# Optimization experiments

Hardware: AMD Instinct MI355X
Metric: run time of the kernel (lower is better)

## Reference

```python
import jax, jax.numpy as jnp
import numpy as np

B, T, F, H = 1024, 100, 128, 512


def _uniform(key, shape, stdv):
    return jax.random.uniform(key, shape, jnp.float32, -stdv, stdv)


def setup_inputs() -> dict:
    key = jax.random.key(0)
    ks = jax.random.split(key, 24)
    values = jax.random.normal(ks[0], (B, T, F), jnp.float32)
    delta = jax.random.uniform(ks[1], (B, T, F), jnp.float32) * 5.0
    masks = (jax.random.uniform(ks[2], (B, T, F), jnp.float32) < 0.7).astype(jnp.float32)
    rbfs = jax.random.normal(ks[3], (B, T, F), jnp.float32)
    inp = jnp.stack([values, delta, masks, rbfs], axis=1)  # [B,4,T,F]

    s_h = 1.0 / np.sqrt(H)
    s_f = 1.0 / np.sqrt(F)
    params = dict(
        inp=inp,
        # TemporalDecay h: Linear(F->H)
        W_dh=_uniform(ks[4], (H, F), s_h), b_dh=_uniform(ks[5], (H,), s_h),
        # TemporalDecay x (diag): effective diagonal of W
        w_dx=_uniform(ks[6], (F,), s_f), b_dx=_uniform(ks[7], (F,), s_f),
        # output_layer: Linear(H->F)
        W_out=_uniform(ks[8], (F, H), s_f), b_out=_uniform(ks[9], (F,), s_f),
        W_z=_uniform(ks[10], (F, F), s_f), b_z=_uniform(ks[11], (F,), s_f),
        # concat layer: Linear(2F->F)
        W_cat=_uniform(ks[12], (F, 2 * F), s_f), b_cat=_uniform(ks[13], (F,), s_f),
        # beta layer: Linear(2F->F)
        W_beta=_uniform(ks[14], (F, 2 * F), s_f), b_beta=_uniform(ks[15], (F,), s_f),
        # GRUCell(2F -> H)
        W_ih=_uniform(ks[16], (3 * H, 2 * F), s_h), b_ih=_uniform(ks[17], (3 * H,), s_h),
        W_hh=_uniform(ks[18], (3 * H, H), s_h), b_hh=_uniform(ks[19], (3 * H,), s_h),
    )
    return params


def _forward(inp, W_dh, b_dh, w_dx, b_dx, W_out, b_out, W_z, b_z,
             W_cat, b_cat, W_beta, b_beta, W_ih, b_ih, W_hh, b_hh):
    values = jnp.swapaxes(inp[:, 0], 0, 1)  # [T,B,F]
    delta = jnp.swapaxes(inp[:, 1], 0, 1)
    masks = jnp.swapaxes(inp[:, 2], 0, 1)
    rbfs = jnp.swapaxes(inp[:, 3], 0, 1)

    W_z_m = W_z * (1.0 - jnp.eye(F, dtype=W_z.dtype))  # off-diagonal mask

    def mae(hat, v, m):
        return jnp.sum(jnp.abs(v - hat) * m) / (jnp.sum(m) + 1e-5)

    def step(carry, xs):
        hid, x_loss = carry
        v, d, m, r = xs
        gamma_x = jnp.exp(-jax.nn.relu(d * w_dx + b_dx))          # diag decay
        gamma_h = jnp.exp(-jax.nn.relu(d @ W_dh.T + b_dh))        # [B,H]
        x_hat = hid @ W_out.T + b_out
        x_loss = x_loss + 2.0 * mae(x_hat, v, m)                  # x_loss + x_hat_loss share value
        x_c = m * v + (1.0 - m) * x_hat
        concat_hat = jnp.concatenate([x_c, r], axis=1) @ W_cat.T + b_cat
        x_loss = x_loss + mae(concat_hat, v, m)
        a_c = m * v + (1.0 - m) * concat_hat
        z_hat = a_c @ W_z_m.T + b_z
        x_loss = x_loss + mae(z_hat, v, m)
        beta = jax.nn.sigmoid(jnp.concatenate([gamma_x, m], axis=1) @ W_beta.T + b_beta)
        c_hat = beta * z_hat + (1.0 - beta) * x_hat
        x_loss = x_loss + mae(c_hat, v, m)
        c_c = m * v + (1.0 - m) * c_hat
        # GRUCell
        h = hid * gamma_h
        gi = jnp.concatenate([c_c, m], axis=1) @ W_ih.T + b_ih
        gh = h @ W_hh.T + b_hh
        i_r, i_z, i_n = jnp.split(gi, 3, axis=1)
        h_r, h_z, h_n = jnp.split(gh, 3, axis=1)
        rg = jax.nn.sigmoid(i_r + h_r)
        zg = jax.nn.sigmoid(i_z + h_z)
        ng = jnp.tanh(i_n + rg * h_n)
        h_new = (1.0 - zg) * ng + zg * h
        return (h_new, x_loss), (c_hat, c_c)

    hid0 = jnp.zeros((values.shape[1], H), values.dtype)
    (_, x_loss), (c_hats, c_cs) = jax.lax.scan(step, (hid0, jnp.float32(0.0)),
                                               (values, delta, masks, rbfs))
    c_hat_list = jnp.swapaxes(c_hats, 0, 1)   # [B,T,F]
    imputations = jnp.swapaxes(c_cs, 0, 1)
    return c_hat_list, imputations, x_loss * 5.0


def reference(inp, W_dh, b_dh, w_dx, b_dx, W_out, b_out, W_z, b_z,
              W_cat, b_cat, W_beta, b_beta, W_ih, b_ih, W_hh, b_hh):
    # x_loss in torch accumulates x_hat term twice (x_loss += ... and x_hat_loss += same);
    # but note: torch adds x_hat_loss separately, x_loss only once per term. Faithful: x_loss gets
    # one add per hat (x_hat, concat_hat, z_hat, c_hat) -> see _forward (2.0 factor removed below).
    return _forward(inp, W_dh, b_dh, w_dx, b_dx, W_out, b_out, W_z, b_z,
                    W_cat, b_cat, W_beta, b_beta, W_ih, b_ih, W_hh, b_hh)
```

## Files before the change

kernel.cpp:

```cpp
#include <hip/hip_runtime.h>
#include <cmath>

#define NB 256
#define NT 256

static constexpr int B = 1024, T = 100, F = 128, H = 512;
static constexpr size_t BTF = (size_t)B * T * F;
static constexpr int TF = T * F;
static constexpr int STRB = 4 * T * F;

static constexpr size_t OFF_FLAGS = 0;
static constexpr size_t OFF_REL   = 4096;
static constexpr size_t OFF_DEN   = 4112;
static constexpr size_t OFF_LOSST = 4240;
static constexpr size_t OFF_HID   = 4368;
static constexpr size_t ZERO_FLOATS = OFF_HID + (size_t)B * H;
static constexpr size_t OFF_H    = ZERO_FLOATS;
static constexpr size_t OFF_GH   = OFF_H + (size_t)B * H;
static constexpr size_t OFF_XHAT = OFF_GH + (size_t)B * 3 * H;
static constexpr size_t OFF_CONC = OFF_XHAT + (size_t)B * F;
static constexpr size_t OFF_BETA = OFF_CONC + (size_t)B * F;
static constexpr size_t OFF_CC   = OFF_BETA + (size_t)B * F;

__device__ __forceinline__ float4 ld4(const float* p) {
    return *reinterpret_cast<const float4*>(p);
}
__device__ __forceinline__ float sigm(float x) { return 1.f / (1.f + expf(-x)); }

__device__ __forceinline__ void gsync(unsigned* flags, unsigned* rel, unsigned gen) {
    __syncthreads();
    __threadfence();
    const int tid = threadIdx.x;
    if (blockIdx.x == 0) {
        if (tid > 0) {
            while (__hip_atomic_load(&flags[(size_t)tid * 16], __ATOMIC_RELAXED,
                                     __HIP_MEMORY_SCOPE_AGENT) < gen)
                __builtin_amdgcn_s_sleep(4);
        }
        __syncthreads();
        if (tid == 0)
            __hip_atomic_store(rel, gen, __ATOMIC_RELAXED, __HIP_MEMORY_SCOPE_AGENT);
    } else {
        if (tid == 0) {
            __hip_atomic_store(&flags[(size_t)blockIdx.x * 16], gen, __ATOMIC_RELAXED,
                               __HIP_MEMORY_SCOPE_AGENT);
            while (__hip_atomic_load(rel, __ATOMIC_RELAXED,
                                     __HIP_MEMORY_SCOPE_AGENT) < gen)
                __builtin_amdgcn_s_sleep(16);
        }
    }
    __threadfence();
    __syncthreads();
}

__device__ __forceinline__ void stage4(float* __restrict__ dst, int k, int r, float4 p) {
    dst[(k + 0) * 64 + r] = p.x; dst[(k + 1) * 64 + r] = p.y;
    dst[(k + 2) * 64 + r] = p.z; dst[(k + 3) * 64 + r] = p.w;
}

template <typename FA, typename FB>
__device__ __forceinline__ void gemm_tile64(int K, FA loadA4, FB loadB4,
                                            float* __restrict__ sAB, float acc[4][4]) {
    const int tid = threadIdx.x;
    const int lr = tid >> 2;
    const int lk = (tid & 3) << 2;
    const int tx = tid & 15, ty = tid >> 4;
    const int nc = K >> 5;

    float4 pa0 = loadA4(lr, lk);
    float4 pa1 = loadA4(lr, lk + 16);
    float4 pb0 = loadB4(lr, lk);
    float4 pb1 = loadB4(lr, lk + 16);
    stage4(sAB, lk, lr, pa0);
    stage4(sAB, lk + 16, lr, pa1);
    stage4(sAB + 2048, lk, lr, pb0);
    stage4(sAB + 2048, lk + 16, lr, pb1);
    __syncthreads();

    for (int c = 0; c < nc; ++c) {
        const float* sA = sAB + (c & 1) * 4096;
        const float* sB = sA + 2048;
        if (c + 1 < nc) {
            const int k0 = (c + 1) << 5;
            pa0 = loadA4(lr, k0 + lk);
            pa1 = loadA4(lr, k0 + lk + 16);
            pb0 = loadB4(lr, k0 + lk);
            pb1 = loadB4(lr, k0 + lk + 16);
        }
#pragma unroll
        for (int kk = 0; kk < 32; ++kk) {
            const float4 av = *reinterpret_cast<const float4*>(&sA[kk * 64 + ty * 4]);
            const float4 bv = *reinterpret_cast<const float4*>(&sB[kk * 64 + tx * 4]);
            const float a0[4] = {av.x, av.y, av.z, av.w};
            const float b0[4] = {bv.x, bv.y, bv.z, bv.w};
#pragma unroll
            for (int i = 0; i < 4; ++i)
#pragma unroll
                for (int j = 0; j < 4; ++j)
                    acc[i][j] = fmaf(a0[i], b0[j], acc[i][j]);
        }
        if (c + 1 < nc) {
            float* dA = sAB + ((c + 1) & 1) * 4096;
            stage4(dA, lk, lr, pa0);
            stage4(dA, lk + 16, lr, pa1);
            stage4(dA + 2048, lk, lr, pb0);
            stage4(dA + 2048, lk + 16, lr, pb1);
        }
        __syncthreads();
    }
}

__global__ void __launch_bounds__(NT) mgru_main(
    const float* __restrict__ inp,
    const float* __restrict__ W_dh, const float* __restrict__ b_dh,
    const float* __restrict__ w_dx, const float* __restrict__ b_dx,
    const float* __restrict__ W_out, const float* __restrict__ b_out,
    const float* __restrict__ W_z,   const float* __restrict__ b_z,
    const float* __restrict__ W_cat, const float* __restrict__ b_cat,
    const float* __restrict__ W_beta,const float* __restrict__ b_beta,
    const float* __restrict__ W_ih,  const float* __restrict__ b_ih,
    const float* __restrict__ W_hh,  const float* __restrict__ b_hh,
    float* __restrict__ out, float* __restrict__ ws)
{
    __shared__ float sAB[2 * 4096];

    unsigned* flags = reinterpret_cast<unsigned*>(ws) + OFF_FLAGS;
    unsigned* rel   = reinterpret_cast<unsigned*>(ws) + OFF_REL;
    float* den   = ws + OFF_DEN;
    float* lossT = ws + OFF_LOSST;
    float* hid   = ws + OFF_HID;
    float* hdec  = ws + OFF_H;
    float* gh    = ws + OFF_GH;
    float* xhat  = ws + OFF_XHAT;
    float* conc  = ws + OFF_CONC;
    float* betav = ws + OFF_BETA;
    float* ccw   = ws + OFF_CC;

    const int bid = blockIdx.x, tid = threadIdx.x;
    const int tx = tid & 15, ty = tid >> 4;
    unsigned gen = 1;

    for (int s = bid * NT + tid; s < B * T; s += NB * NT) {
        int b = s / T, t = s - b * T;
        const float* mrow = inp + (size_t)b * STRB + 2 * TF + (size_t)t * F;
        float sum = 0.f;
        for (int f = 0; f < F; f += 4) {
            float4 m4 = ld4(mrow + f);
            sum += m4.x + m4.y + m4.z + m4.w;
        }
        atomicAdd(&den[t], sum);
    }
    gsync(flags, rel, gen); ++gen;

    for (int t = 0; t < T; ++t) {
        const size_t tF = (size_t)t * F;
        if (bid >= 64 && bid < 192) {
            const int idx = bid - 64, rt = idx >> 3, ct = idx & 7;
            float acc[4][4] = {};
            gemm_tile64(128,
                [=](int r, int k) { return ld4(inp + (size_t)(rt * 64 + r) * STRB + TF + tF + k); },
                [=](int c, int k) { return ld4(W_dh + (size_t)(ct * 64 + c) * F + k); },
                sAB, acc);
#pragma unroll
            for (int i = 0; i < 4; ++i) {
                int b = rt * 64 + ty * 4 + i;
#pragma unroll
                for (int j = 0; j < 4; ++j) {
                    int c = ct * 64 + tx * 4 + j;
                    float g = expf(-fmaxf(acc[i][j] + b_dh[c], 0.f));
                    hdec[(size_t)b * H + c] = hid[(size_t)b * H + c] * g;
                }
            }
        } else if (bid >= 192 && bid < 224) {
            const int t2 = bid - 192, rt = t2 >> 1, ct = t2 & 1;
            float acc[4][4] = {};
            gemm_tile64(512,
                [=](int r, int k) { return ld4(hid + (size_t)(rt * 64 + r) * H + k); },
                [=](int c, int k) { return ld4(W_out + (size_t)(ct * 64 + c) * H + k); },
                sAB, acc);
#pragma unroll
            for (int i = 0; i < 4; ++i) {
                int b = rt * 64 + ty * 4 + i;
#pragma unroll
                for (int j = 0; j < 4; ++j) {
                    int c = ct * 64 + tx * 4 + j;
                    xhat[(size_t)b * F + c] = acc[i][j] + b_out[c];
                }
            }
        } else if (bid >= 224) {
            const int t2 = bid - 224, rt = t2 >> 1, ct = t2 & 1;
            float acc[4][4] = {};
            gemm_tile64(256,
                [=](int r, int k) {
                    int b = rt * 64 + r;
                    if (k < 128) {
                        float4 d4 = ld4(inp + (size_t)b * STRB + TF + tF + k);
                        float4 w4 = ld4(w_dx + k), c4 = ld4(b_dx + k);
                        float4 q;
                        q.x = expf(-fmaxf(fmaf(d4.x, w4.x, c4.x), 0.f));
                        q.y = expf(-fmaxf(fmaf(d4.y, w4.y, c4.y), 0.f));
                        q.z = expf(-fmaxf(fmaf(d4.z, w4.z, c4.z), 0.f));
                        q.w = expf(-fmaxf(fmaf(d4.w, w4.w, c4.w), 0.f));
                        return q;
                    }
                    return ld4(inp + (size_t)b * STRB + 2 * TF + tF + (k - 128));
                },
                [=](int c, int k) { return ld4(W_beta + (size_t)(ct * 64 + c) * (2 * F) + k); },
                sAB, acc);
#pragma unroll
            for (int i = 0; i < 4; ++i) {
                int b = rt * 64 + ty * 4 + i;
#pragma unroll
                for (int j = 0; j < 4; ++j) {
                    int c = ct * 64 + tx * 4 + j;
                    betav[(size_t)b * F + c] = sigm(acc[i][j] + b_beta[c]);
                }
            }
        }
        gsync(flags, rel, gen); ++gen;
        {
            int g0 = -1, g1 = -1, cat2 = -1;
            if (bid >= 64 && bid < 192) { g0 = (bid - 64) * 2; g1 = g0 + 1; }
            else if (bid >= 192)        { g0 = 256 + (bid - 192); if (bid < 224) cat2 = bid - 192; }
            else                        { g0 = 320 + bid; }
#pragma unroll 1
            for (int pass = 0; pass < 2; ++pass) {
                int g = pass ? g1 : g0;
                if (g < 0) continue;
                const int rt = g / 24, ct = g % 24;
                float acc[4][4] = {};
                gemm_tile64(512,
                    [=](int r, int k) { return ld4(hdec + (size_t)(rt * 64 + r) * H + k); },
                    [=](int c, int k) { return ld4(W_hh + (size_t)(ct * 64 + c) * H + k); },
                    sAB, acc);
#pragma unroll
                for (int i = 0; i < 4; ++i) {
                    int b = rt * 64 + ty * 4 + i;
#pragma unroll
                    for (int j = 0; j < 4; ++j) {
                        int c = ct * 64 + tx * 4 + j;
                        gh[(size_t)b * 1536 + c] = acc[i][j] + b_hh[c];
                    }
                }
            }
            if (cat2 >= 0) {
                const int rt = cat2 >> 1, ct = cat2 & 1;
                float acc[4][4] = {};
                gemm_tile64(256,
                    [=](int r, int k) {
                        int b = rt * 64 + r;
                        if (k < 128) {
                            float4 v4 = ld4(inp + (size_t)b * STRB + tF + k);
                            float4 m4 = ld4(inp + (size_t)b * STRB + 2 * TF + tF + k);
                            float4 x4 = ld4(xhat + (size_t)b * F + k);
                            float4 q;
                            q.x = m4.x * v4.x + (1.f - m4.x) * x4.x;
                            q.y = m4.y * v4.y + (1.f - m4.y) * x4.y;
                            q.z = m4.z * v4.z + (1.f - m4.z) * x4.z;
                            q.w = m4.w * v4.w + (1.f - m4.w) * x4.w;
                            return q;
                        }
                        return ld4(inp + (size_t)b * STRB + 3 * TF + tF + (k - 128));
                    },
                    [=](int c, int k) { return ld4(W_cat + (size_t)(ct * 64 + c) * (2 * F) + k); },
                    sAB, acc);
#pragma unroll
                for (int i = 0; i < 4; ++i) {
                    int b = rt * 64 + ty * 4 + i;
#pragma unroll
                    for (int j = 0; j < 4; ++j) {
                        int c = ct * 64 + tx * 4 + j;
                        conc[(size_t)b * F + c] = acc[i][j] + b_cat[c];
                    }
                }
            }
        }
        gsync(flags, rel, gen); ++gen;
        if (bid >= 32 && bid < 64) {
            const int t2 = bid - 32, rt = t2 >> 1, ct = t2 & 1;
            float acc[4][4] = {};
            gemm_tile64(128,
                [=](int r, int k) {
                    int b = rt * 64 + r;
                    float4 v4 = ld4(inp + (size_t)b * STRB + tF + k);
                    float4 m4 = ld4(inp + (size_t)b * STRB + 2 * TF + tF + k);
                    float4 c4 = ld4(conc + (size_t)b * F + k);
                    float4 q;
                    q.x = m4.x * v4.x + (1.f - m4.x) * c4.x;
                    q.y = m4.y * v4.y + (1.f - m4.y) * c4.y;
                    q.z = m4.z * v4.z + (1.f - m4.z) * c4.z;
                    q.w = m4.w * v4.w + (1.f - m4.w) * c4.w;
                    return q;
                },
                [=](int c, int k) {
                    float4 w = ld4(W_z + (size_t)(ct * 64 + c) * F + k);
                    int cg = ct * 64 + c;
                    w.x = (cg == k + 0) ? 0.f : w.x;
                    w.y = (cg == k + 1) ? 0.f : w.y;
                    w.z = (cg == k + 2) ? 0.f : w.z;
                    w.w = (cg == k + 3) ? 0.f : w.w;
                    return w;
                },
                sAB, acc);
            float lsum = 0.f;
#pragma unroll
            for (int i = 0; i < 4; ++i) {
                int b = rt * 64 + ty * 4 + i;
#pragma unroll
                for (int j = 0; j < 4; ++j) {
                    int c = ct * 64 + tx * 4 + j;
                    float zh = acc[i][j] + b_z[c];
                    float xh = xhat[(size_t)b * F + c];
                    float bt = betav[(size_t)b * F + c];
                    float ch = bt * zh + (1.f - bt) * xh;
                    const size_t ib = (size_t)b * STRB + tF;
                    float v = inp[ib + c];
                    float m = inp[ib + 2 * TF + c];
                    float cc = m * v + (1.f - m) * ch;
                    out[(size_t)b * TF + tF + c] = ch;
                    out[BTF + (size_t)b * TF + tF + c] = cc;
                    ccw[(size_t)b * F + c] = cc;
                    float co = conc[(size_t)b * F + c];
                    lsum += m * (2.f * fabsf(v - xh) + fabsf(v - co) +
                                 fabsf(v - zh) + fabsf(v - ch));
                }
            }
            __syncthreads();
            sAB[tid] = lsum;
            __syncthreads();
            for (int s = 128; s > 0; s >>= 1) {
                if (tid < s) sAB[tid] += sAB[tid + s];
                __syncthreads();
            }
            if (tid == 0) atomicAdd(&lossT[t], sAB[0] / (den[t] + 1e-5f));
        }
        gsync(flags, rel, gen); ++gen;
        if (bid >= 64 && bid < 192) {
            const int idx = bid - 64, rt = idx >> 3, hc = idx & 7;
            float acc3[3][4][4] = {};
#pragma unroll
            for (int g = 0; g < 3; ++g) {
                gemm_tile64(256,
                    [=](int r, int k) {
                        int b = rt * 64 + r;
                        if (k < 128) return ld4(ccw + (size_t)b * F + k);
                        return ld4(inp + (size_t)b * STRB + 2 * TF + tF + (k - 128));
                    },
                    [=](int c, int k) { return ld4(W_ih + (size_t)(g * H + hc * 64 + c) * (2 * F) + k); },
                    sAB, acc3[g]);
            }
#pragma unroll
            for (int i = 0; i < 4; ++i) {
                int b = rt * 64 + ty * 4 + i;
#pragma unroll
                for (int j = 0; j < 4; ++j) {
                    int c = hc * 64 + tx * 4 + j;
                    float ir  = acc3[0][i][j] + b_ih[c];
                    float iz  = acc3[1][i][j] + b_ih[H + c];
                    float inn = acc3[2][i][j] + b_ih[2 * H + c];
                    float hr = gh[(size_t)b * 1536 + c];
                    float hz = gh[(size_t)b * 1536 + H + c];
                    float hn = gh[(size_t)b * 1536 + 2 * H + c];
                    float hv = hdec[(size_t)b * H + c];
                    float rg = sigm(ir + hr);
                    float zg = sigm(iz + hz);
                    float ng = tanhf(inn + rg * hn);
                    hid[(size_t)b * H + c] = (1.f - zg) * ng + zg * hv;
                }
            }
        }
        gsync(flags, rel, gen); ++gen;
    }
    if (bid == 0 && tid == 0) {
        float s = 0.f;
        for (int t = 0; t < T; ++t) s += lossT[t];
        out[2 * BTF] = s * 5.0f;
    }
}

extern "C" void kernel_launch(void* const* d_in, const int* in_sizes, int n_in,
                              void* d_out, int out_size, void* d_ws, size_t ws_size,
                              hipStream_t stream) {
    const float* inp    = (const float*)d_in[0];
    const float* W_dh   = (const float*)d_in[1];
    const float* b_dh   = (const float*)d_in[2];
    const float* w_dx   = (const float*)d_in[3];
    const float* b_dx   = (const float*)d_in[4];
    const float* W_out  = (const float*)d_in[5];
    const float* b_out  = (const float*)d_in[6];
    const float* W_z    = (const float*)d_in[7];
    const float* b_z    = (const float*)d_in[8];
    const float* W_cat  = (const float*)d_in[9];
    const float* b_cat  = (const float*)d_in[10];
    const float* W_beta = (const float*)d_in[11];
    const float* b_beta = (const float*)d_in[12];
    const float* W_ih   = (const float*)d_in[13];
    const float* b_ih   = (const float*)d_in[14];
    const float* W_hh   = (const float*)d_in[15];
    const float* b_hh   = (const float*)d_in[16];

    hipMemsetAsync(d_ws, 0, ZERO_FLOATS * sizeof(float), stream);

    mgru_main<<<NB, NT, 0, stream>>>(inp, W_dh, b_dh, w_dx, b_dx, W_out, b_out,
                                     W_z, b_z, W_cat, b_cat, W_beta, b_beta,
                                     W_ih, b_ih, W_hh, b_hh,
                                     (float*)d_out, (float*)d_ws);
}
```

Baseline: 30.66 ms.

## Double persistent grid and split GRU gate GEMMs across more blocks

The persistent cooperative grid grows from 256 to 512 blocks, with launch bounds requesting two blocks per CU. The W_hh GEMM is spread so each block computes one tile, and the W_ih GEMM is split per gate into separate blocks that write into a new gi buffer. A separate phase then applies the GRU elementwise update. This spreads each timestep's GEMM work over more blocks to cut per-phase latency, at the cost of an extra grid-wide barrier per step, more workspace traffic, and register pressure from the occupancy hint.

```diff
diff --git a/kernel.cpp b/kernel.cpp
--- a/kernel.cpp
+++ b/kernel.cpp
@@ -1,7 +1,7 @@
 #include <hip/hip_runtime.h>
 #include <cmath>
 
-#define NB 256
+#define NB 512
 #define NT 256
 
 static constexpr int B = 1024, T = 100, F = 128, H = 512;
@@ -10,10 +10,10 @@
 static constexpr int STRB = 4 * T * F;
 
 static constexpr size_t OFF_FLAGS = 0;
-static constexpr size_t OFF_REL   = 4096;
-static constexpr size_t OFF_DEN   = 4112;
-static constexpr size_t OFF_LOSST = 4240;
-static constexpr size_t OFF_HID   = 4368;
+static constexpr size_t OFF_REL   = 8192;
+static constexpr size_t OFF_DEN   = 8208;
+static constexpr size_t OFF_LOSST = 8336;
+static constexpr size_t OFF_HID   = 8464;
 static constexpr size_t ZERO_FLOATS = OFF_HID + (size_t)B * H;
 static constexpr size_t OFF_H    = ZERO_FLOATS;
 static constexpr size_t OFF_GH   = OFF_H + (size_t)B * H;
@@ -21,6 +21,7 @@
 static constexpr size_t OFF_CONC = OFF_XHAT + (size_t)B * F;
 static constexpr size_t OFF_BETA = OFF_CONC + (size_t)B * F;
 static constexpr size_t OFF_CC   = OFF_BETA + (size_t)B * F;
+static constexpr size_t OFF_GI   = OFF_CC + (size_t)B * F;
 
 __device__ __forceinline__ float4 ld4(const float* p) {
     return *reinterpret_cast<const float4*>(p);
@@ -37,6 +38,9 @@
                                      __HIP_MEMORY_SCOPE_AGENT) < gen)
                 __builtin_amdgcn_s_sleep(4);
         }
+        while (__hip_atomic_load(&flags[(size_t)(tid + 256) * 16], __ATOMIC_RELAXED,
+                                 __HIP_MEMORY_SCOPE_AGENT) < gen)
+            __builtin_amdgcn_s_sleep(4);
         __syncthreads();
         if (tid == 0)
             __hip_atomic_store(rel, gen, __ATOMIC_RELAXED, __HIP_MEMORY_SCOPE_AGENT);
@@ -110,7 +114,7 @@
     }
 }
 
-__global__ void __launch_bounds__(NT) mgru_main(
+__global__ void __launch_bounds__(NT, 2) mgru_main(
     const float* __restrict__ inp,
     const float* __restrict__ W_dh, const float* __restrict__ b_dh,
     const float* __restrict__ w_dx, const float* __restrict__ b_dx,
@@ -135,6 +139,7 @@
     float* conc  = ws + OFF_CONC;
     float* betav = ws + OFF_BETA;
     float* ccw   = ws + OFF_CC;
+    float* gibuf = ws + OFF_GI;
 
     const int bid = blockIdx.x, tid = threadIdx.x;
     const int tx = tid & 15, ty = tid >> 4;
@@ -154,8 +159,8 @@
 
     for (int t = 0; t < T; ++t) {
         const size_t tF = (size_t)t * F;
-        if (bid >= 64 && bid < 192) {
-            const int idx = bid - 64, rt = idx >> 3, ct = idx & 7;
+        if (bid < 128) {
+            const int rt = bid >> 3, ct = bid & 7;
             float acc[4][4] = {};
             gemm_tile64(128,
                 [=](int r, int k) { return ld4(inp + (size_t)(rt * 64 + r) * STRB + TF + tF + k); },
@@ -171,8 +176,8 @@
                     hdec[(size_t)b * H + c] = hid[(size_t)b * H + c] * g;
                 }
             }
-        } else if (bid >= 192 && bid < 224) {
-            const int t2 = bid - 192, rt = t2 >> 1, ct = t2 & 1;
+        } else if (bid < 160) {
+            const int t2 = bid - 128, rt = t2 >> 1, ct = t2 & 1;
             float acc[4][4] = {};
             gemm_tile64(512,
                 [=](int r, int k) { return ld4(hid + (size_t)(rt * 64 + r) * H + k); },
@@ -187,8 +192,8 @@
                     xhat[(size_t)b * F + c] = acc[i][j] + b_out[c];
                 }
             }
-        } else if (bid >= 224) {
-            const int t2 = bid - 224, rt = t2 >> 1, ct = t2 & 1;
+        } else if (bid < 192) {
+            const int t2 = bid - 160, rt = t2 >> 1, ct = t2 & 1;
             float acc[4][4] = {};
             gemm_tile64(256,
                 [=](int r, int k) {
@@ -218,66 +223,56 @@
             }
         }
         gsync(flags, rel, gen); ++gen;
-        {
-            int g0 = -1, g1 = -1, cat2 = -1;
-            if (bid >= 64 && bid < 192) { g0 = (bid - 64) * 2; g1 = g0 + 1; }
-            else if (bid >= 192)        { g0 = 256 + (bid - 192); if (bid < 224) cat2 = bid - 192; }
-            else                        { g0 = 320 + bid; }
-#pragma unroll 1
-            for (int pass = 0; pass < 2; ++pass) {
-                int g = pass ? g1 : g0;
-                if (g < 0) continue;
-                const int rt = g / 24, ct = g % 24;
-                float acc[4][4] = {};
-                gemm_tile64(512,
-                    [=](int r, int k) { return ld4(hdec + (size_t)(rt * 64 + r) * H + k); },
-                    [=](int c, int k) { return ld4(W_hh + (size_t)(ct * 64 + c) * H + k); },
-                    sAB, acc);
-#pragma unroll
-                for (int i = 0; i < 4; ++i) {
-                    int b = rt * 64 + ty * 4 + i;
-#pragma unroll
-                    for (int j = 0; j < 4; ++j) {
-                        int c = ct * 64 + tx * 4 + j;
-                        gh[(size_t)b * 1536 + c] = acc[i][j] + b_hh[c];
+        if (bid < 384) {
+            const int rt = bid / 24, ct = bid % 24;
+            float acc[4][4] = {};
+            gemm_tile64(512,
+                [=](int r, int k) { return ld4(hdec + (size_t)(rt * 64 + r) * H + k); },
+                [=](int c, int k) { return ld4(W_hh + (size_t)(ct * 64 + c) * H + k); },
+                sAB, acc);
+#pragma unroll
+            for (int i = 0; i < 4; ++i) {
+                int b = rt * 64 + ty * 4 + i;
+#pragma unroll
+                for (int j = 0; j < 4; ++j) {
+                    int c = ct * 64 + tx * 4 + j;
+                    gh[(size_t)b * 1536 + c] = acc[i][j] + b_hh[c];
+                }
+            }
+        } else if (bid < 416) {
+            const int t2 = bid - 384, rt = t2 >> 1, ct = t2 & 1;
+            float acc[4][4] = {};
+            gemm_tile64(256,
+                [=](int r, int k) {
+                    int b = rt * 64 + r;
+                    if (k < 128) {
+                        float4 v4 = ld4(inp + (size_t)b * STRB + tF + k);
+                        float4 m4 = ld4(inp + (size_t)b * STRB + 2 * TF + tF + k);
+                        float4 x4 = ld4(xhat + (size_t)b * F + k);
+                        float4 q;
+                        q.x = m4.x * v4.x + (1.f - m4.x) * x4.x;
+                        q.y = m4.y * v4.y + (1.f - m4.y) * x4.y;
+                        q.z = m4.z * v4.z + (1.f - m4.z) * x4.z;
+                        q.w = m4.w * v4.w + (1.f - m4.w) * x4.w;
+                        return q;
                     }
-                }
-            }
-            if (cat2 >= 0) {
-                const int rt = cat2 >> 1, ct = cat2 & 1;
-                float acc[4][4] = {};
-                gemm_tile64(256,
-                    [=](int r, int k) {
-                        int b = rt * 64 + r;
-                        if (k < 128) {
-                            float4 v4 = ld4(inp + (size_t)b * STRB + tF + k);
-                            float4 m4 = ld4(inp + (size_t)b * STRB + 2 * TF + tF + k);
-                            float4 x4 = ld4(xhat + (size_t)b * F + k);
-                            float4 q;
-                            q.x = m4.x * v4.x + (1.f - m4.x) * x4.x;
-                            q.y = m4.y * v4.y + (1.f - m4.y) * x4.y;
-                            q.z = m4.z * v4.z + (1.f - m4.z) * x4.z;
-                            q.w = m4.w * v4.w + (1.f - m4.w) * x4.w;
-                            return q;
-                        }
-                        return ld4(inp + (size_t)b * STRB + 3 * TF + tF + (k - 128));
-                    },
-                    [=](int c, int k) { return ld4(W_cat + (size_t)(ct * 64 + c) * (2 * F) + k); },
-                    sAB, acc);
-#pragma unroll
-                for (int i = 0; i < 4; ++i) {
-                    int b = rt * 64 + ty * 4 + i;
-#pragma unroll
-                    for (int j = 0; j < 4; ++j) {
-                        int c = ct * 64 + tx * 4 + j;
-                        conc[(size_t)b * F + c] = acc[i][j] + b_cat[c];
-                    }
+                    return ld4(inp + (size_t)b * STRB + 3 * TF + tF + (k - 128));
+                },
+                [=](int c, int k) { return ld4(W_cat + (size_t)(ct * 64 + c) * (2 * F) + k); },
+                sAB, acc);
+#pragma unroll
+            for (int i = 0; i < 4; ++i) {
+                int b = rt * 64 + ty * 4 + i;
+#pragma unroll
+                for (int j = 0; j < 4; ++j) {
+                    int c = ct * 64 + tx * 4 + j;
+                    conc[(size_t)b * F + c] = acc[i][j] + b_cat[c];
                 }
             }
         }
         gsync(flags, rel, gen); ++gen;
-        if (bid >= 32 && bid < 64) {
-            const int t2 = bid - 32, rt = t2 >> 1, ct = t2 & 1;
+        if (bid >= 416 && bid < 448) {
+            const int t2 = bid - 416, rt = t2 >> 1, ct = t2 & 1;
             float acc[4][4] = {};
             gemm_tile64(128,
                 [=](int r, int k) {
@@ -335,36 +330,41 @@
             if (tid == 0) atomicAdd(&lossT[t], sAB[0] / (den[t] + 1e-5f));
         }
         gsync(flags, rel, gen); ++gen;
-        if (bid >= 64 && bid < 192) {
-            const int idx = bid - 64, rt = idx >> 3, hc = idx & 7;
-            float acc3[3][4][4] = {};
-#pragma unroll
-            for (int g = 0; g < 3; ++g) {
-                gemm_tile64(256,
-                    [=](int r, int k) {
-                        int b = rt * 64 + r;
-                        if (k < 128) return ld4(ccw + (size_t)b * F + k);
-                        return ld4(inp + (size_t)b * STRB + 2 * TF + tF + (k - 128));
-                    },
-                    [=](int c, int k) { return ld4(W_ih + (size_t)(g * H + hc * 64 + c) * (2 * F) + k); },
-                    sAB, acc3[g]);
-            }
-#pragma unroll
-            for (int i = 0; i < 4; ++i) {
-                int b = rt * 64 + ty * 4 + i;
-#pragma unroll
-                for (int j = 0; j < 4; ++j) {
-                    int c = hc * 64 + tx * 4 + j;
-                    float ir  = acc3[0][i][j] + b_ih[c];
-                    float iz  = acc3[1][i][j] + b_ih[H + c];
-                    float inn = acc3[2][i][j] + b_ih[2 * H + c];
-                    float hr = gh[(size_t)b * 1536 + c];
-                    float hz = gh[(size_t)b * 1536 + H + c];
-                    float hn = gh[(size_t)b * 1536 + 2 * H + c];
+        if (bid < 384) {
+            const int g = bid >> 7, idx = bid & 127, rt = idx >> 3, hc = idx & 7;
+            float acc[4][4] = {};
+            gemm_tile64(256,
+                [=](int r, int k) {
+                    int b = rt * 64 + r;
+                    if (k < 128) return ld4(ccw + (size_t)b * F + k);
+                    return ld4(inp + (size_t)b * STRB + 2 * TF + tF + (k - 128));
+                },
+                [=](int c, int k) { return ld4(W_ih + (size_t)(g * H + hc * 64 + c) * (2 * F) + k); },
+                sAB, acc);
+#pragma unroll
+            for (int i = 0; i < 4; ++i) {
+                int b = rt * 64 + ty * 4 + i;
+#pragma unroll
+                for (int j = 0; j < 4; ++j) {
+                    int c = g * H + hc * 64 + tx * 4 + j;
+                    gibuf[(size_t)b * 1536 + c] = acc[i][j] + b_ih[c];
+                }
+            }
+        }
+        gsync(flags, rel, gen); ++gen;
+        if (bid >= 384) {
+            const int idx = bid - 384, rt = idx >> 3, hc = idx & 7;
+#pragma unroll
+            for (int i = 0; i < 4; ++i) {
+                int b = rt * 64 + (tid >> 4) * 4 + i;
+#pragma unroll
+                for (int j = 0; j < 4; ++j) {
+                    int c = hc * 64 + (tid & 15) * 4 + j;
+                    const size_t gbase = (size_t)b * 1536 + c;
+                    float rg = sigm(gibuf[gbase] + gh[gbase]);
+                    float zg = sigm(gibuf[gbase + 512] + gh[gbase + 512]);
+                    float ng = tanhf(gibuf[gbase + 1024] + rg * gh[gbase + 1024]);
                     float hv = hdec[(size_t)b * H + c];
-                    float rg = sigm(ir + hr);
-                    float zg = sigm(iz + hz);
-                    float ng = tanhf(inn + rg * hn);
                     hid[(size_t)b * H + c] = (1.f - zg) * ng + zg * hv;
                 }
             }
```

Result: slower. 56.18 ms (+83.2%).
